# Kernel optimization log

Hardware: AMD Instinct MI355X
Metric: run time of the kernel (lower is better)

## Reference

```python
import jax, jax.numpy as jnp
import numpy as np

N_NODES = 100000
N_EDGES = 400000
N_GRAPHS = 4000
IN_DIM = 128
HID = 512
N_DESC = 200
N_CLASSES = 2


def setup_inputs() -> dict:
    key = jax.random.key(0)
    ks = jax.random.split(key, 16)
    features = jax.random.normal(ks[0], (N_NODES, IN_DIM), jnp.float32)
    descriptors = jax.random.normal(ks[1], (N_GRAPHS, N_DESC), jnp.float32)
    src = jax.random.randint(ks[2], (N_EDGES,), 0, N_NODES)
    dst = jax.random.randint(ks[3], (N_EDGES,), 0, N_NODES)
    node2graph = jnp.sort(jax.random.randint(ks[4], (N_NODES,), 0, N_GRAPHS))

    def unif(k, shape, fan_out):
        stdv = 1.0 / np.sqrt(fan_out)
        return jax.random.uniform(k, shape, jnp.float32, -stdv, stdv)

    # GCN layer params (torch init: uniform(-1/sqrt(out), 1/sqrt(out)))
    W1 = unif(ks[5], (IN_DIM, HID), HID)
    b1 = unif(ks[6], (HID,), HID)
    W2 = unif(ks[7], (HID, HID), HID)
    b2 = unif(ks[8], (HID,), HID)
    # MLP head (torch Linear default init: uniform(-1/sqrt(fan_in), ...))
    lw1 = unif(ks[9], (HID + N_DESC, 500), HID + N_DESC)
    lb1 = unif(ks[10], (500,), HID + N_DESC)
    lw2 = unif(ks[11], (500, 100), 500)
    lb2 = unif(ks[12], (100,), 500)
    cw = unif(ks[13], (100, N_CLASSES), 100)
    cb = unif(ks[14], (N_CLASSES,), 100)
    return {"features": features, "descriptors": descriptors, "src": src,
            "dst": dst, "node2graph": node2graph, "W1": W1, "b1": b1,
            "W2": W2, "b2": b2, "lw1": lw1, "lb1": lb1, "lw2": lw2,
            "lb2": lb2, "cw": cw, "cb": cb}


def reference(features, descriptors, src, dst, node2graph,
              W1, b1, W2, b2, lw1, lb1, lw2, lb2, cw, cb):
    N = features.shape[0]
    B = descriptors.shape[0]

    def gcn(h, W, b):
        hW = h @ W                                    # [N, F_out]
        # copy_src + sum: gather source features per edge, scatter-sum to dst
        agg = jax.ops.segment_sum(hW[src], dst, num_segments=N)
        return jax.nn.relu(agg + b)

    h = gcn(features, W1, b1)                         # dropout skipped (eval)
    h = gcn(h, W2, b2)

    # dgl.mean_nodes: per-graph mean over nodes
    sums = jax.ops.segment_sum(h, node2graph, num_segments=B)     # [B, HID]
    counts = jax.ops.segment_sum(jnp.ones((N,), h.dtype), node2graph,
                                 num_segments=B)
    hg = sums / jnp.maximum(counts, 1.0)[:, None]

    x = jnp.concatenate([hg, descriptors], axis=1)    # [B, HID+N_DESC]
    x = jax.nn.relu(x @ lw1 + lb1)
    x = jax.nn.relu(x @ lw2 + lb2)
    return x @ cw + cb                                # [B, n_classes]
```

## Files before the change

### kernel.cpp

```cpp
#include <hip/hip_runtime.h>
#include <hip/hip_bf16.h>

#define N_NODES  100000
#define N_EDGES  400000
#define N_GRAPHS 4000
#define IN_DIM   128
#define HID      512
#define N_DESC   200
#define N_CLASSES 2
#define MLP1_OUT 500
#define MLP2_OUT 100
#define XIN_DIM  (HID + N_DESC)
#define XIN_PAD  768

#define SCAN_CHUNK 1024
#define NCHK ((N_NODES + SCAN_CHUNK - 1) / SCAN_CHUNK)

typedef __hip_bfloat16  bf16;
typedef __hip_bfloat162 bf16x2;
typedef short s8v  __attribute__((ext_vector_type(8)));
typedef float f32x4 __attribute__((ext_vector_type(4)));

__device__ __forceinline__ float ldf(const float* p, size_t i) { return p[i]; }
__device__ __forceinline__ float ldf(const bf16* p, size_t i)  { return __bfloat162float(p[i]); }

__device__ __forceinline__ short f2bs(float x) {
    bf16 h = __float2bfloat16(x);
    return __builtin_bit_cast(short, h);
}

__device__ __forceinline__ void gld16(const short* g, short* l) {
    __builtin_amdgcn_global_load_lds(
        (const __attribute__((address_space(1))) unsigned int*)g,
        (__attribute__((address_space(3))) unsigned int*)l, 16, 0, 0);
}

#define MEMFENCE asm volatile("" ::: "memory")

__global__ __launch_bounds__(256)
void detect_dtype_kernel(const unsigned* __restrict__ words, unsigned nw,
                         int* __restrict__ flag)
{
    __shared__ int s_cnt;
    if (threadIdx.x == 0) s_cnt = 0;
    __syncthreads();
    const int SAMPLES = 2048;
    int sane = 0;
    for (int i = threadIdx.x; i < SAMPLES; i += 256) {
        size_t idx = (size_t)(((unsigned long long)i * 2654435761ull) % nw);
        unsigned w = words[idx];
        float f = __uint_as_float((w & 0xFFFFu) << 16);
        float a = fabsf(f);
        if (f == 0.0f || (a > 1e-8f && a < 1e8f)) sane++;
    }
    atomicAdd(&s_cnt, sane);
    __syncthreads();
    if (threadIdx.x == 0) *flag = (s_cnt * 10 > SAMPLES * 6) ? 1 : 0;
}

template<typename FT>
__device__ __forceinline__
void prep_body(int i, const FT* W1, const FT* W2, const FT* lw1, const FT* lw2,
               const FT* b1, const FT* b2, const FT* lb1, const FT* lb2,
               short* W1t, short* W2t, short* lw1t, short* lw2t,
               float* b1f, float* b2f, float* lb1f, float* lb2f)
{
    if (i < 65536) {
        int n = i >> 7, k = i & 127;
        W1t[i] = f2bs(ldf(W1, (size_t)k * HID + n));
        return;
    }
    i -= 65536;
    if (i < 262144) {
        int n = i >> 9, k = i & 511;
        W2t[i] = f2bs(ldf(W2, (size_t)k * HID + n));
        return;
    }
    i -= 262144;
    if (i < 393216) {
        int n = i / XIN_PAD, k = i - n * XIN_PAD;
        lw1t[i] = (n < MLP1_OUT && k < XIN_DIM)
                      ? f2bs(ldf(lw1, (size_t)k * MLP1_OUT + n)) : (short)0;
        return;
    }
    i -= 393216;
    if (i < 65536) {
        int n = i >> 9, k = i & 511;
        lw2t[i] = (n < MLP2_OUT && k < MLP1_OUT)
                      ? f2bs(ldf(lw2, (size_t)k * MLP2_OUT + n)) : (short)0;
        return;
    }
    i -= 65536;
    if (i < 512) { b1f[i] = ldf(b1, i); return; }
    i -= 512;
    if (i < 512) { b2f[i] = ldf(b2, i); return; }
    i -= 512;
    if (i < 512) { lb1f[i] = (i < MLP1_OUT) ? ldf(lb1, i) : 0.f; return; }
    i -= 512;
    if (i < 128) { lb2f[i] = (i < MLP2_OUT) ? ldf(lb2, i) : 0.f; return; }
}

__global__ __launch_bounds__(256)
void prep_weights_kernel(const void* __restrict__ W1, const void* __restrict__ W2,
                         const void* __restrict__ lw1, const void* __restrict__ lw2,
                         const void* __restrict__ b1, const void* __restrict__ b2,
                         const void* __restrict__ lb1, const void* __restrict__ lb2,
                         short* __restrict__ W1t, short* __restrict__ W2t,
                         short* __restrict__ lw1t, short* __restrict__ lw2t,
                         float* __restrict__ b1f, float* __restrict__ b2f,
                         float* __restrict__ lb1f, float* __restrict__ lb2f,
                         const int* __restrict__ flag)
{
    int i = blockIdx.x * 256 + threadIdx.x;
    if (*flag == 0)
        prep_body<float>(i, (const float*)W1, (const float*)W2, (const float*)lw1,
                         (const float*)lw2, (const float*)b1, (const float*)b2,
                         (const float*)lb1, (const float*)lb2,
                         W1t, W2t, lw1t, lw2t, b1f, b2f, lb1f, lb2f);
    else
        prep_body<bf16>(i, (const bf16*)W1, (const bf16*)W2, (const bf16*)lw1,
                        (const bf16*)lw2, (const bf16*)b1, (const bf16*)b2,
                        (const bf16*)lb1, (const bf16*)lb2,
                        W1t, W2t, lw1t, lw2t, b1f, b2f, lb1f, lb2f);
}

__global__ __launch_bounds__(256)
void deg_kernel(const int* __restrict__ dst, int* __restrict__ deg)
{
    int e = blockIdx.x * 256 + threadIdx.x;
    if (e < N_EDGES) atomicAdd(&deg[dst[e]], 1);
}

__global__ __launch_bounds__(256)
void scan_partial_kernel(const int* __restrict__ deg, int* __restrict__ part)
{
    int c = blockIdx.x, t = threadIdx.x;
    int i0 = c * SCAN_CHUNK + t * 4;
    int s = 0;
#pragma unroll
    for (int j = 0; j < 4; j++) {
        int i = i0 + j;
        if (i < N_NODES) s += deg[i];
    }
    __shared__ int red[256];
    red[t] = s;
    __syncthreads();
    for (int off = 128; off > 0; off >>= 1) {
        if (t < off) red[t] += red[t + off];
        __syncthreads();
    }
    if (t == 0) part[c] = red[0];
}

__global__ void scan_parts_kernel(int* __restrict__ part, int* __restrict__ edge_start)
{
    int run = 0;
    for (int c = 0; c < NCHK; c++) { int v = part[c]; part[c] = run; run += v; }
    edge_start[N_NODES] = run;
}

__global__ __launch_bounds__(256)
void scan_final_kernel(const int* __restrict__ deg, const int* __restrict__ part,
                       int* __restrict__ edge_start, int* __restrict__ cursor)
{
    int c = blockIdx.x, t = threadIdx.x;
    int i0 = c * SCAN_CHUNK + t * 4;
    int d[4];
    int tsum = 0;
#pragma unroll
    for (int j = 0; j < 4; j++) {
        int i = i0 + j;
        d[j] = (i < N_NODES) ? deg[i] : 0;
        tsum += d[j];
    }
    __shared__ int s[256];
    s[t] = tsum;
    __syncthreads();
    for (int off = 1; off < 256; off <<= 1) {
        int v = (t >= off) ? s[t - off] : 0;
        __syncthreads();
        s[t] += v;
        __syncthreads();
    }
    int run = part[c] + s[t] - tsum;
#pragma unroll
    for (int j = 0; j < 4; j++) {
        int i = i0 + j;
        if (i < N_NODES) { edge_start[i] = run; cursor[i] = run; run += d[j]; }
    }
}

__global__ __launch_bounds__(256)
void fill_kernel(const int* __restrict__ src, const int* __restrict__ dst,
                 int* __restrict__ cursor, int* __restrict__ csr_src)
{
    int e = blockIdx.x * 256 + threadIdx.x;
    if (e >= N_EDGES) return;
    int p = atomicAdd(&cursor[dst[e]], 1);
    csr_src[p] = src[e];
}

__global__ __launch_bounds__(256)
void gstart_kernel(const int* __restrict__ n2g, int* __restrict__ gstart)
{
    int n = blockIdx.x * 256 + threadIdx.x;
    if (n > N_NODES) return;
    if (n == N_NODES) {
        int last = n2g[N_NODES - 1];
        for (int g = last + 1; g <= N_GRAPHS; g++) gstart[g] = N_NODES;
        return;
    }
    int v = n2g[n];
    int prev = (n == 0) ? -1 : n2g[n - 1];
    for (int g = prev + 1; g <= v; g++) gstart[g] = n;
}

__global__ __launch_bounds__(256)
void gather_feat_kernel(const void* __restrict__ feat_, const int* __restrict__ edge_start,
                        const int* __restrict__ csr_src, bf16* __restrict__ agg1,
                        const int* __restrict__ flag)
{
    int n = blockIdx.x * 4 + (threadIdx.x >> 6);
    if (n >= N_NODES) return;
    int lane = threadIdx.x & 63;
    int e0 = edge_start[n], e1 = edge_start[n + 1];
    float2 acc = {0.f, 0.f};
    if (*flag == 0) {
        const float* feat = (const float*)feat_;
        for (int i = e0; i < e1; i++) {
            int s = csr_src[i];
            float2 f = ((const float2*)(feat + (size_t)s * IN_DIM))[lane];
            acc.x += f.x; acc.y += f.y;
        }
    } else {
        const bf16* feat = (const bf16*)feat_;
        for (int i = e0; i < e1; i++) {
            int s = csr_src[i];
            float2 f = __bfloat1622float2(((const bf16x2*)(feat + (size_t)s * IN_DIM))[lane]);
            acc.x += f.x; acc.y += f.y;
        }
    }
    bf16x2 p;
    p.x = __float2bfloat16(acc.x);
    p.y = __float2bfloat16(acc.y);
    ((bf16x2*)(agg1 + (size_t)n * IN_DIM))[lane] = p;
}

__global__ __launch_bounds__(256)
void gather_h_kernel(const bf16* __restrict__ h1, const int* __restrict__ edge_start,
                     const int* __restrict__ csr_src, bf16* __restrict__ aggc)
{
    int n = blockIdx.x * 4 + (threadIdx.x >> 6);
    if (n >= N_NODES) return;
    int lane = threadIdx.x & 63;
    int e0 = edge_start[n], e1 = edge_start[n + 1];
    float acc[8];
#pragma unroll
    for (int j = 0; j < 8; j++) acc[j] = 0.f;
    for (int i = e0; i < e1; i++) {
        int s = csr_src[i];
        float4 r = ((const float4*)(h1 + (size_t)s * HID))[lane];
        const bf16x2* p = (const bf16x2*)&r;
#pragma unroll
        for (int q = 0; q < 4; q++) {
            float2 f = __bfloat1622float2(p[q]);
            acc[2 * q] += f.x; acc[2 * q + 1] += f.y;
        }
    }
    s8v s;
#pragma unroll
    for (int j = 0; j < 8; j++) s[j] = f2bs(acc[j]);
    ((float4*)(aggc + (size_t)n * HID))[lane] = __builtin_bit_cast(float4, s);
}

template<int NCT>
__global__ __launch_bounds__(256, 4)
void mfma_gemm_kernel(const short* __restrict__ A, const short* __restrict__ Bt,
                      const float* __restrict__ biasf, bf16* __restrict__ Cout,
                      int M, int K, int nrt)
{
    __shared__ short smem[17408];
    short* Cs = smem;

    const int b  = blockIdx.x;
    const int r8 = b & 7;
    const int t0 = b >> 3;
    const int x  = (t0 / NCT) * 8 + r8;
    const int y  = t0 % NCT;
    if (x >= nrt) return;
    const int row0 = x * 128;
    const int col0 = y * 128;

    const int tid  = threadIdx.x;
    const int lane = tid & 63;
    const int w    = tid >> 6;
    const int wr = w >> 1, wc = w & 1;
    const int m  = lane & 15, q = lane >> 4;

    const int rr = lane >> 2;
    const int dc = ((lane & 3) ^ ((lane >> 3) & 3)) * 8;
    const short* pA = A  + (size_t)(row0 + w * 32 + rr) * K + dc;
    const short* pB = Bt + (size_t)(col0 + w * 32 + rr) * K + dc;
    const int cOff = 16 * K;

    const int so = (q ^ ((m >> 1) & 3)) * 8;

    f32x4 acc[4][4];
#pragma unroll
    for (int i = 0; i < 4; i++)
#pragma unroll
        for (int j = 0; j < 4; j++) acc[i][j] = {0.f, 0.f, 0.f, 0.f};

    {
        short* d = smem + w * 1024;
        gld16(pA, d);               gld16(pA + cOff, d + 512);
        gld16(pB, d + 4096);        gld16(pB + cOff, d + 4096 + 512);
        pA += 32; pB += 32;
    }

    const int NT = K >> 5;
    for (int t = 0; t < NT; ++t) {
        const int boff = (t & 1) << 13;
        if (t + 1 < NT) {
            short* d = smem + (8192 - boff) + w * 1024;
            gld16(pA, d);           gld16(pA + cOff, d + 512);
            gld16(pB, d + 4096);    gld16(pB + cOff, d + 4096 + 512);
            pA += 32; pB += 32;
            asm volatile("s_waitcnt vmcnt(4)" ::: "memory");
        } else {
            asm volatile("s_waitcnt vmcnt(0)" ::: "memory");
        }
        __builtin_amdgcn_s_barrier();
        MEMFENCE;

        const short* Ab = smem + boff;
        const short* Bb = smem + boff + 4096;
        s8v av[4], bv[4];
#pragma unroll
        for (int rt = 0; rt < 4; rt++)
            av[rt] = *(const s8v*)&Ab[(wr * 64 + rt * 16 + m) * 32 + so];
#pragma unroll
        for (int ct = 0; ct < 4; ct++)
            bv[ct] = *(const s8v*)&Bb[(wc * 64 + ct * 16 + m) * 32 + so];
#pragma unroll
        for (int rt = 0; rt < 4; rt++)
#pragma unroll
            for (int ct = 0; ct < 4; ct++)
                acc[rt][ct] = __builtin_amdgcn_mfma_f32_16x16x32_bf16(
                    av[rt], bv[ct], acc[rt][ct], 0, 0, 0);

        MEMFENCE;
        __builtin_amdgcn_s_barrier();
        MEMFENCE;
    }

#pragma unroll
    for (int rt = 0; rt < 4; rt++) {
#pragma unroll
        for (int ct = 0; ct < 4; ct++) {
            int lcol = wc * 64 + ct * 16 + m;
            float bv = biasf[col0 + lcol];
#pragma unroll
            for (int reg = 0; reg < 4; reg++) {
                int lrow = wr * 64 + rt * 16 + q * 4 + reg;
                float v = acc[rt][ct][reg] + bv;
                v = v > 0.f ? v : 0.f;
                Cs[lrow * 136 + lcol] = f2bs(v);
            }
        }
    }
    __syncthreads();

#pragma unroll
    for (int it = 0; it < 8; it++) {
        int idx = it * 256 + tid;
        int r = idx >> 4;
        int c = (idx & 15) * 8;
        int row = row0 + r;
        if (row < M)
            *(float4*)&Cout[(size_t)row * HID + col0 + c] =
                *(const float4*)&Cs[r * 136 + c];
    }
}

__global__ __launch_bounds__(256)
void pool_graph_kernel(const bf16* __restrict__ h2, const int* __restrict__ gstart,
                       float* __restrict__ hg)
{
    int g = blockIdx.x * 4 + (threadIdx.x >> 6);
    if (g >= N_GRAPHS) return;
    int lane = threadIdx.x & 63;
    int s0 = gstart[g], s1 = gstart[g + 1];
    float acc[8];
#pragma unroll
    for (int j = 0; j < 8; j++) acc[j] = 0.f;
    for (int n = s0; n < s1; n++) {
        float4 r = ((const float4*)(h2 + (size_t)n * HID))[lane];
        const bf16x2* p = (const bf16x2*)&r;
#pragma unroll
        for (int q = 0; q < 4; q++) {
            float2 f = __bfloat1622float2(p[q]);
            acc[2 * q] += f.x; acc[2 * q + 1] += f.y;
        }
    }
    float* orow = hg + (size_t)g * HID + lane * 8;
    ((float4*)orow)[0] = make_float4(acc[0], acc[1], acc[2], acc[3]);
    ((float4*)orow)[1] = make_float4(acc[4], acc[5], acc[6], acc[7]);
}

__global__ __launch_bounds__(256)
void build_xin_kernel(const float* __restrict__ hg, const int* __restrict__ gstart,
                      const void* __restrict__ desc_, bf16* __restrict__ xinb,
                      const int* __restrict__ flag)
{
    int idx = blockIdx.x * 256 + threadIdx.x;
    if (idx >= N_GRAPHS * XIN_PAD) return;
    int g = idx / XIN_PAD;
    int c = idx - g * XIN_PAD;
    float v;
    if (c < HID) {
        float cnt = (float)(gstart[g + 1] - gstart[g]);
        v = hg[(size_t)g * HID + c] / (cnt > 1.0f ? cnt : 1.0f);
    } else if (c < XIN_DIM) {
        size_t di = (size_t)g * N_DESC + (c - HID);
        v = (*flag == 0) ? ((const float*)desc_)[di]
                         : __bfloat162float(((const bf16*)desc_)[di]);
    } else {
        v = 0.f;
    }
    xinb[idx] = __float2bfloat16(v);
}

__global__ __launch_bounds__(256)
void final_layer_kernel(const bf16* __restrict__ x2b, const void* __restrict__ cw_,
                        const void* __restrict__ cb_, void* __restrict__ out_,
                        const int* __restrict__ flag)
{
    int i = blockIdx.x * 256 + threadIdx.x;
    if (i >= N_GRAPHS * N_CLASSES) return;
    int r = i >> 1, c = i & 1;
    const bf16* x = x2b + (size_t)r * HID;
    if (*flag == 0) {
        const float* cw = (const float*)cw_;
        float acc = ((const float*)cb_)[c];
#pragma unroll 4
        for (int k = 0; k < MLP2_OUT; k++)
            acc += __bfloat162float(x[k]) * cw[k * N_CLASSES + c];
        ((float*)out_)[i] = acc;
    } else {
        const bf16* cw = (const bf16*)cw_;
        float acc = __bfloat162float(((const bf16*)cb_)[c]);
#pragma unroll 4
        for (int k = 0; k < MLP2_OUT; k++)
            acc += __bfloat162float(x[k]) * __bfloat162float(cw[k * N_CLASSES + c]);
        ((bf16*)out_)[i] = __float2bfloat16(acc);
    }
}

static inline size_t align_up(size_t x, size_t a) { return (x + a - 1) & ~(a - 1); }
static inline int swgrid(int nrt, int nct) { return ((nrt + 7) / 8) * 8 * nct; }

extern "C" void kernel_launch(void* const* d_in, const int* in_sizes, int n_in,
                              void* d_out, int out_size, void* d_ws, size_t ws_size,
                              hipStream_t stream)
{
    const void* features    = d_in[0];
    const void* descriptors = d_in[1];
    const int*  src         = (const int*)d_in[2];
    const int*  dst         = (const int*)d_in[3];
    const int*  node2graph  = (const int*)d_in[4];
    const void* W1          = d_in[5];
    const void* b1          = d_in[6];
    const void* W2          = d_in[7];
    const void* b2          = d_in[8];
    const void* lw1         = d_in[9];
    const void* lb1         = d_in[10];
    const void* lw2         = d_in[11];
    const void* lb2         = d_in[12];
    const void* cw          = d_in[13];
    const void* cb          = d_in[14];
    (void)in_sizes; (void)n_in; (void)out_size; (void)ws_size;

    char* ws = (char*)d_ws;
    size_t off = 0;
    bf16* agg1 = (bf16*)(ws + off);
    bf16* aggc = (bf16*)(ws + off);
    bf16* xinb = (bf16*)(ws + off);
    bf16* x1b  = (bf16*)(ws + off + (size_t)8 * 1024 * 1024);
    bf16* x2b  = (bf16*)(ws + off + (size_t)16 * 1024 * 1024);
    off = align_up(off + (size_t)N_NODES * HID * sizeof(bf16), 256);
    bf16* h1 = (bf16*)(ws + off);
    bf16* h2 = (bf16*)(ws + off);
    off = align_up(off + (size_t)N_NODES * HID * sizeof(bf16), 256);
    float* hg = (float*)(ws + off);
    off = align_up(off + (size_t)N_GRAPHS * HID * sizeof(float), 256);
    int* dflag = (int*)(ws + off);          off = align_up(off + 256, 256);
    int* edge_start = (int*)(ws + off);     off = align_up(off + (N_NODES + 1) * 4, 256);
    int* cursor = (int*)(ws + off);         off = align_up(off + N_NODES * 4, 256);
    int* csr_src = (int*)(ws + off);        off = align_up(off + N_EDGES * 4, 256);
    int* part = (int*)(ws + off);           off = align_up(off + NCHK * 4, 256);
    int* deg = (int*)(ws + off);            off = align_up(off + N_NODES * 4, 256);
    int* gstart = (int*)(ws + off);         off = align_up(off + (N_GRAPHS + 1) * 4, 256);
    short* W1t  = (short*)(ws + off);       off = align_up(off + (size_t)HID * IN_DIM * 2, 256);
    short* W2t  = (short*)(ws + off);       off = align_up(off + (size_t)HID * HID * 2, 256);
    short* lw1t = (short*)(ws + off);       off = align_up(off + (size_t)512 * XIN_PAD * 2, 256);
    short* lw2t = (short*)(ws + off);       off = align_up(off + (size_t)128 * HID * 2, 256);
    float* b1f  = (float*)(ws + off);       off = align_up(off + 512 * 4, 256);
    float* b2f  = (float*)(ws + off);       off = align_up(off + 512 * 4, 256);
    float* lb1f = (float*)(ws + off);       off = align_up(off + 512 * 4, 256);
    float* lb2f = (float*)(ws + off);       off = align_up(off + 128 * 4, 256);

    detect_dtype_kernel<<<1, 256, 0, stream>>>(
        (const unsigned*)features, (unsigned)(N_NODES * IN_DIM / 2), dflag);

    {
        int nblk = (788096 + 255) / 256;
        prep_weights_kernel<<<nblk, 256, 0, stream>>>(
            W1, W2, lw1, lw2, b1, b2, lb1, lb2,
            W1t, W2t, lw1t, lw2t, b1f, b2f, lb1f, lb2f, dflag);
    }

    hipMemsetAsync(deg, 0, N_NODES * 4, stream);
    deg_kernel<<<(N_EDGES + 255) / 256, 256, 0, stream>>>(dst, deg);
    scan_partial_kernel<<<NCHK, 256, 0, stream>>>(deg, part);
    scan_parts_kernel<<<1, 1, 0, stream>>>(part, edge_start);
    scan_final_kernel<<<NCHK, 256, 0, stream>>>(deg, part, edge_start, cursor);
    fill_kernel<<<(N_EDGES + 255) / 256, 256, 0, stream>>>(src, dst, cursor, csr_src);
    gstart_kernel<<<(N_NODES + 256) / 256, 256, 0, stream>>>(node2graph, gstart);

    gather_feat_kernel<<<N_NODES / 4, 256, 0, stream>>>(
        features, edge_start, csr_src, agg1, dflag);
    {
        int nrt = (N_NODES + 127) / 128;
        mfma_gemm_kernel<4><<<swgrid(nrt, 4), 256, 0, stream>>>(
            (const short*)agg1, W1t, b1f, h1, N_NODES, IN_DIM, nrt);
    }

    gather_h_kernel<<<N_NODES / 4, 256, 0, stream>>>(h1, edge_start, csr_src, aggc);
    {
        int nrt = (N_NODES + 127) / 128;
        mfma_gemm_kernel<4><<<swgrid(nrt, 4), 256, 0, stream>>>(
            (const short*)aggc, W2t, b2f, h2, N_NODES, HID, nrt);
    }
    pool_graph_kernel<<<N_GRAPHS / 4, 256, 0, stream>>>(h2, gstart, hg);

    {
        int nthr = (N_GRAPHS * XIN_PAD + 255) / 256;
        build_xin_kernel<<<nthr, 256, 0, stream>>>(
            hg, gstart, descriptors, xinb, dflag);
    }
    {
        int nrt = (N_GRAPHS + 127) / 128;
        mfma_gemm_kernel<4><<<swgrid(nrt, 4), 256, 0, stream>>>(
            (const short*)xinb, lw1t, lb1f, x1b, N_GRAPHS, XIN_PAD, nrt);
    }
    {
        int nrt = (N_GRAPHS + 127) / 128;
        mfma_gemm_kernel<1><<<swgrid(nrt, 1), 256, 0, stream>>>(
            (const short*)x1b, lw2t, lb2f, x2b, N_GRAPHS, HID, nrt);
    }
    {
        int nthr = (N_GRAPHS * N_CLASSES + 255) / 256;
        final_layer_kernel<<<nthr, 256, 0, stream>>>(
            x2b, cw, cb, d_out, dflag);
    }
}
```

Baseline: 452.1 us.

## Reorder layer-2 GEMM before aggregation and fuse gather with graph pooling

Applies the second GCN weight matrix before neighbour aggregation, so the GEMM writes an unactivated projection. A new kernel then gathers neighbour rows per node, adds bias and ReLU, and accumulates directly into per-graph sums. This removes the separate gather pass and the materialised layer-2 output along with their memory traffic. In exchange, the fused kernel parallelises only over graphs, so each wave processes many nodes and edges serially with much lower occupancy.

Result: slower. 473.2 us (+4.7%).

```diff
diff --git a/kernel.cpp b/kernel.cpp
--- a/kernel.cpp
+++ b/kernel.cpp
@@ -246,34 +246,7 @@
     ((bf16x2*)(agg1 + (size_t)n * IN_DIM))[lane] = p;
 }
 
-__global__ __launch_bounds__(256)
-void gather_h_kernel(const bf16* __restrict__ h1, const int* __restrict__ edge_start,
-                     const int* __restrict__ csr_src, bf16* __restrict__ aggc)
-{
-    int n = blockIdx.x * 4 + (threadIdx.x >> 6);
-    if (n >= N_NODES) return;
-    int lane = threadIdx.x & 63;
-    int e0 = edge_start[n], e1 = edge_start[n + 1];
-    float acc[8];
-#pragma unroll
-    for (int j = 0; j < 8; j++) acc[j] = 0.f;
-    for (int i = e0; i < e1; i++) {
-        int s = csr_src[i];
-        float4 r = ((const float4*)(h1 + (size_t)s * HID))[lane];
-        const bf16x2* p = (const bf16x2*)&r;
-#pragma unroll
-        for (int q = 0; q < 4; q++) {
-            float2 f = __bfloat1622float2(p[q]);
-            acc[2 * q] += f.x; acc[2 * q + 1] += f.y;
-        }
-    }
-    s8v s;
-#pragma unroll
-    for (int j = 0; j < 8; j++) s[j] = f2bs(acc[j]);
-    ((float4*)(aggc + (size_t)n * HID))[lane] = __builtin_bit_cast(float4, s);
-}
-
-template<int NCT>
+template<int NCT, int ACT>
 __global__ __launch_bounds__(256, 4)
 void mfma_gemm_kernel(const short* __restrict__ A, const short* __restrict__ Bt,
                       const float* __restrict__ biasf, bf16* __restrict__ Cout,
@@ -359,12 +332,15 @@
 #pragma unroll
         for (int ct = 0; ct < 4; ct++) {
             int lcol = wc * 64 + ct * 16 + m;
-            float bv = biasf[col0 + lcol];
+            float bv = ACT ? biasf[col0 + lcol] : 0.f;
 #pragma unroll
             for (int reg = 0; reg < 4; reg++) {
                 int lrow = wr * 64 + rt * 16 + q * 4 + reg;
-                float v = acc[rt][ct][reg] + bv;
-                v = v > 0.f ? v : 0.f;
+                float v = acc[rt][ct][reg];
+                if constexpr (ACT) {
+                    v += bv;
+                    v = v > 0.f ? v : 0.f;
+                }
                 Cs[lrow * 136 + lcol] = f2bs(v);
             }
         }
@@ -384,28 +360,52 @@
 }
 
 __global__ __launch_bounds__(256)
-void pool_graph_kernel(const bf16* __restrict__ h2, const int* __restrict__ gstart,
-                       float* __restrict__ hg)
+void gather_pool_kernel(const bf16* __restrict__ G, const int* __restrict__ edge_start,
+                        const int* __restrict__ csr_src, const int* __restrict__ gstart,
+                        const float* __restrict__ b2f, float* __restrict__ hg)
 {
     int g = blockIdx.x * 4 + (threadIdx.x >> 6);
     if (g >= N_GRAPHS) return;
     int lane = threadIdx.x & 63;
+
+    float bj[8];
+    {
+        const float4* bp = (const float4*)(b2f + lane * 8);
+        float4 b0 = bp[0], b1 = bp[1];
+        bj[0] = b0.x; bj[1] = b0.y; bj[2] = b0.z; bj[3] = b0.w;
+        bj[4] = b1.x; bj[5] = b1.y; bj[6] = b1.z; bj[7] = b1.w;
+    }
+
     int s0 = gstart[g], s1 = gstart[g + 1];
-    float acc[8];
-#pragma unroll
-    for (int j = 0; j < 8; j++) acc[j] = 0.f;
-    for (int n = s0; n < s1; n++) {
-        float4 r = ((const float4*)(h2 + (size_t)n * HID))[lane];
-        const bf16x2* p = (const bf16x2*)&r;
-#pragma unroll
-        for (int q = 0; q < 4; q++) {
-            float2 f = __bfloat1622float2(p[q]);
-            acc[2 * q] += f.x; acc[2 * q + 1] += f.y;
+    float hacc[8];
+#pragma unroll
+    for (int j = 0; j < 8; j++) hacc[j] = 0.f;
+
+    for (int n = s0; n < s1; ++n) {
+        int e0 = edge_start[n], e1 = edge_start[n + 1];
+        float racc[8];
+#pragma unroll
+        for (int j = 0; j < 8; j++) racc[j] = 0.f;
+        for (int e = e0; e < e1; ++e) {
+            int s = csr_src[e];
+            float4 r = ((const float4*)(G + (size_t)s * HID))[lane];
+            const bf16x2* p = (const bf16x2*)&r;
+#pragma unroll
+            for (int qq = 0; qq < 4; qq++) {
+                float2 f = __bfloat1622float2(p[qq]);
+                racc[2 * qq] += f.x; racc[2 * qq + 1] += f.y;
+            }
         }
-    }
+#pragma unroll
+        for (int j = 0; j < 8; j++) {
+            float v = racc[j] + bj[j];
+            hacc[j] += (v > 0.f ? v : 0.f);
+        }
+    }
+
     float* orow = hg + (size_t)g * HID + lane * 8;
-    ((float4*)orow)[0] = make_float4(acc[0], acc[1], acc[2], acc[3]);
-    ((float4*)orow)[1] = make_float4(acc[4], acc[5], acc[6], acc[7]);
+    ((float4*)orow)[0] = make_float4(hacc[0], hacc[1], hacc[2], hacc[3]);
+    ((float4*)orow)[1] = make_float4(hacc[4], hacc[5], hacc[6], hacc[7]);
 }
 
 __global__ __launch_bounds__(256)
@@ -484,13 +484,12 @@
     char* ws = (char*)d_ws;
     size_t off = 0;
     bf16* agg1 = (bf16*)(ws + off);
-    bf16* aggc = (bf16*)(ws + off);
+    bf16* G    = (bf16*)(ws + off);
     bf16* xinb = (bf16*)(ws + off);
     bf16* x1b  = (bf16*)(ws + off + (size_t)8 * 1024 * 1024);
     bf16* x2b  = (bf16*)(ws + off + (size_t)16 * 1024 * 1024);
     off = align_up(off + (size_t)N_NODES * HID * sizeof(bf16), 256);
     bf16* h1 = (bf16*)(ws + off);
-    bf16* h2 = (bf16*)(ws + off);
     off = align_up(off + (size_t)N_NODES * HID * sizeof(bf16), 256);
     float* hg = (float*)(ws + off);
     off = align_up(off + (size_t)N_GRAPHS * HID * sizeof(float), 256);
@@ -532,17 +531,17 @@
         features, edge_start, csr_src, agg1, dflag);
     {
         int nrt = (N_NODES + 127) / 128;
-        mfma_gemm_kernel<4><<<swgrid(nrt, 4), 256, 0, stream>>>(
+        mfma_gemm_kernel<4, 1><<<swgrid(nrt, 4), 256, 0, stream>>>(
             (const short*)agg1, W1t, b1f, h1, N_NODES, IN_DIM, nrt);
     }
 
-    gather_h_kernel<<<N_NODES / 4, 256, 0, stream>>>(h1, edge_start, csr_src, aggc);
     {
         int nrt = (N_NODES + 127) / 128;
-        mfma_gemm_kernel<4><<<swgrid(nrt, 4), 256, 0, stream>>>(
-            (const short*)aggc, W2t, b2f, h2, N_NODES, HID, nrt);
-    }
-    pool_graph_kernel<<<N_GRAPHS / 4, 256, 0, stream>>>(h2, gstart, hg);
+        mfma_gemm_kernel<4, 0><<<swgrid(nrt, 4), 256, 0, stream>>>(
+            (const short*)h1, W2t, b2f , G, N_NODES, HID, nrt);
+    }
+    gather_pool_kernel<<<N_GRAPHS / 4, 256, 0, stream>>>(
+        G, edge_start, csr_src, gstart, b2f, hg);
 
     {
         int nthr = (N_GRAPHS * XIN_PAD + 255) / 256;
@@ -551,12 +550,12 @@
     }
     {
         int nrt = (N_GRAPHS + 127) / 128;
-        mfma_gemm_kernel<4><<<swgrid(nrt, 4), 256, 0, stream>>>(
+        mfma_gemm_kernel<4, 1><<<swgrid(nrt, 4), 256, 0, stream>>>(
             (const short*)xinb, lw1t, lb1f, x1b, N_GRAPHS, XIN_PAD, nrt);
     }
     {
         int nrt = (N_GRAPHS + 127) / 128;
-        mfma_gemm_kernel<1><<<swgrid(nrt, 1), 256, 0, stream>>>(
+        mfma_gemm_kernel<1, 1><<<swgrid(nrt, 1), 256, 0, stream>>>(
             (const short*)x1b, lw2t, lb2f, x2b, N_GRAPHS, HID, nrt);
     }
     {
```
